# Performance work log

Measured on AMD Instinct MI355X. Metric: run time of the kernel, lower is better.

Reference implementation:

```python
import jax, jax.numpy as jnp
import numpy as np

N = 50000          # nodes
E = 800000         # edges (before self-loops)
NIN = 300          # n_in
H = 4              # heads
C = 64             # nhid (per-head out channels)
G = 256            # number of graphs in batch
NOUT = 768         # nout
NEG_SLOPE_ATT = 0.2   # PyG GATConv leaky-relu slope for attention logits
NEG_SLOPE_ACT = 0.01  # nn.LeakyReLU default


def setup_inputs() -> dict:
    key = jax.random.key(0)
    ks = jax.random.split(key, 9)
    x = jax.random.normal(ks[0], (N, NIN), dtype=jnp.float32)
    edge_index = jax.random.randint(ks[1], (2, E), 0, N, dtype=jnp.int32)
    batch = jnp.sort(jax.random.randint(ks[2], (N,), 0, G, dtype=jnp.int32))
    lin_w = jax.random.normal(ks[3], (NIN, H * C), dtype=jnp.float32) / np.sqrt(NIN)
    att_src = jax.random.normal(ks[4], (H, C), dtype=jnp.float32) / np.sqrt(C)
    att_dst = jax.random.normal(ks[5], (H, C), dtype=jnp.float32) / np.sqrt(C)
    bias = jnp.zeros((H * C,), dtype=jnp.float32)
    fc1_w = jax.random.normal(ks[6], (H * C, NOUT), dtype=jnp.float32) / np.sqrt(H * C)
    fc1_b = jnp.zeros((NOUT,), dtype=jnp.float32)
    return {"x": x, "edge_index": edge_index, "batch": batch, "lin_w": lin_w,
            "att_src": att_src, "att_dst": att_dst, "bias": bias,
            "fc1_w": fc1_w, "fc1_b": fc1_b}


def reference(x, edge_index, batch, lin_w, att_src, att_dst, bias, fc1_w, fc1_b):
    n = x.shape[0]
    h = (x @ lin_w).reshape(n, H, C)                      # [N,H,C]
    # add self-loops (PyG GATConv default)
    loop = jnp.arange(n, dtype=edge_index.dtype)
    src = jnp.concatenate([edge_index[0], loop])          # [E+N]
    dst = jnp.concatenate([edge_index[1], loop])
    # per-edge attention logits
    a_src = jnp.einsum('nhc,hc->nh', h, att_src)          # [N,H]
    a_dst = jnp.einsum('nhc,hc->nh', h, att_dst)
    e = jax.nn.leaky_relu(a_src[src] + a_dst[dst], NEG_SLOPE_ATT)  # [E+N,H]
    # segment softmax grouped by destination node (self-loops -> every segment nonempty)
    emax = jax.ops.segment_max(e, dst, num_segments=n)    # [N,H]
    ee = jnp.exp(e - emax[dst])
    denom = jax.ops.segment_sum(ee, dst, num_segments=n)
    alpha = ee / denom[dst]                               # [E+N,H]
    # weighted message aggregation
    msg = h[src] * alpha[..., None]                       # [E+N,H,C]
    out = jax.ops.segment_sum(msg, dst, num_segments=n).reshape(n, H * C) + bias
    out = jax.nn.leaky_relu(out, NEG_SLOPE_ACT)
    # global mean pool over graphs
    sums = jax.ops.segment_sum(out, batch, num_segments=G)        # [G,H*C]
    cnt = jax.ops.segment_sum(jnp.ones((n, 1), out.dtype), batch, num_segments=G)
    pooled = sums / jnp.maximum(cnt, 1.0)
    return pooled @ fc1_w + fc1_b                         # [G,NOUT]
```

## Files before the change

kernel.cpp:

```cpp
#include <hip/hip_runtime.h>
#include <hip/hip_bf16.h>

using bf16 = __hip_bfloat16;
typedef __attribute__((ext_vector_type(8))) short short8;
typedef __attribute__((ext_vector_type(4))) float f32x4;

constexpr int N   = 50000;
constexpr int E   = 800000;
constexpr int NIN = 300;
constexpr int H   = 4;
constexpr int C   = 64;
constexpr int HC  = H * C;
constexpr int G   = 256;
constexpr int NOUT = 768;
constexpr int NKB = 10;
constexpr int NT  = 782;
constexpr int DCAP = 64;
constexpr int SCB  = (E + 255) / 256;

__device__ __forceinline__ float b2f(bf16 v) { return __bfloat162float(v); }
__device__ __forceinline__ float us2f(unsigned short u) {
    bf16 b; *(unsigned short*)&b = u; return __bfloat162float(b);
}
__device__ __forceinline__ unsigned short f2us(float f) {
    bf16 b = __float2bfloat16(f); return *(unsigned short*)&b;
}
__device__ __forceinline__ float lrelu_att(float v) { return v > 0.f ? v : 0.2f * v; }
__device__ __forceinline__ float lrelu_act(float v) { return v > 0.f ? v : 0.01f * v; }
__device__ __forceinline__ float ldin(const void* p, int isbf, size_t i) {
    return isbf ? b2f(((const bf16*)p)[i]) : ((const float*)p)[i];
}
__device__ __forceinline__ short8 pack8u(ushort4 lo, ushort4 hi) {
    short8 r;
    r[0] = (short)lo.x; r[1] = (short)lo.y; r[2] = (short)lo.z; r[3] = (short)lo.w;
    r[4] = (short)hi.x; r[5] = (short)hi.y; r[6] = (short)hi.z; r[7] = (short)hi.w;
    return r;
}
__device__ __forceinline__ short8 pack8f(float4 lo, float4 hi) {
    short8 r;
    r[0] = (short)f2us(lo.x); r[1] = (short)f2us(lo.y); r[2] = (short)f2us(lo.z); r[3] = (short)f2us(lo.w);
    r[4] = (short)f2us(hi.x); r[5] = (short)f2us(hi.y); r[6] = (short)f2us(hi.z); r[7] = (short)f2us(hi.w);
    return r;
}

__device__ __forceinline__ short8 loadA_bf(const unsigned short* __restrict__ xr, int kb, int q) {
    ushort4 z = make_ushort4(0, 0, 0, 0);
    ushort4 lo = z, hi = z;
    if (kb < 9) {
        lo = *(const ushort4*)(xr + kb * 32);
        hi = *(const ushort4*)(xr + kb * 32 + 4);
    } else if (q == 0) {
        lo = *(const ushort4*)(xr + 288); hi = *(const ushort4*)(xr + 292);
    } else if (q == 1) {
        lo = *(const ushort4*)(xr + 288);
    }
    return pack8u(lo, hi);
}
__device__ __forceinline__ short8 loadA_f32(const float* __restrict__ xf, int kb, int q) {
    float4 zf = make_float4(0.f, 0.f, 0.f, 0.f);
    float4 lo = zf, hi = zf;
    if (kb < 9) {
        lo = *(const float4*)(xf + kb * 32);
        hi = *(const float4*)(xf + kb * 32 + 4);
    } else if (q == 0) {
        lo = *(const float4*)(xf + 288); hi = *(const float4*)(xf + 292);
    } else if (q == 1) {
        lo = *(const float4*)(xf + 288);
    }
    return pack8f(lo, hi);
}

__device__ __forceinline__ int block_detect(const unsigned short* __restrict__ xr) {
    __shared__ int cnt_s;
    if (threadIdx.x == 0) cnt_s = 0;
    __syncthreads();
    unsigned short u = xr[threadIdx.x & 255];
    int ex = (u >> 7) & 0xFF;
    int ok = (ex == 0) || (ex >= 100 && ex <= 140);
    if (threadIdx.x < 256) atomicAdd(&cnt_s, ok);
    __syncthreads();
    return (cnt_s >= 240) ? 1 : 0;
}

__global__ __launch_bounds__(256) void k_pre(const unsigned short* __restrict__ xr,
                                             const void* __restrict__ w,
                                             const int* __restrict__ batch,
                                             int* __restrict__ flag,
                                             unsigned short* __restrict__ bswz,
                                             int* __restrict__ gs,
                                             const int* __restrict__ ei,
                                             int* __restrict__ cnt,
                                             int* __restrict__ csrB) {
    int b = blockIdx.x;
    if (b < 40) {
        int isbf = block_detect(xr);
        if (b == 0 && threadIdx.x == 0) *flag = isbf;
        int fb = b * 4 + (threadIdx.x >> 6);
        if (fb < 160) {
            int kb = fb >> 4, nb = fb & 15;
            int lane = threadIdx.x & 63;
            int q = lane >> 4, cl = lane & 15;
            int n = nb * 16 + cl;
            unsigned short v[8];
#pragma unroll
            for (int j = 0; j < 8; j++) {
                int k = kb * 32 + q * 8 + j;
                float f = (k < NIN) ? ldin(w, isbf, (size_t)k * HC + n) : 0.f;
                v[j] = f2us(f);
            }
            ushort4* dst = (ushort4*)(bswz + ((size_t)fb * 64 + lane) * 8);
            dst[0] = make_ushort4(v[0], v[1], v[2], v[3]);
            dst[1] = make_ushort4(v[4], v[5], v[6], v[7]);
        }
    } else if (b == 40) {
        int g = threadIdx.x;
        int lo = 0, hi = N;
        while (lo < hi) {
            int mid = (lo + hi) >> 1;
            if (batch[mid] < g) lo = mid + 1;
            else hi = mid;
        }
        gs[g] = lo;
        if (g == 0) gs[G] = N;
    } else {
        int e = (b - 41) * 256 + threadIdx.x;
        if (e < E) {
            int s = ei[e], d = ei[E + e];
            int pos = atomicAdd(&cnt[d], 1);
            if (pos < DCAP) csrB[(size_t)d * DCAP + pos] = s;
        }
    }
}

__global__ __launch_bounds__(256, 4) void k_lin4(const void* __restrict__ x,
                                                 const unsigned short* __restrict__ bswz,
                                                 const void* __restrict__ att_s,
                                                 const void* __restrict__ att_d,
                                                 unsigned short* __restrict__ hb,
                                                 float* __restrict__ a_src,
                                                 float* __restrict__ a_dst,
                                                 const int* __restrict__ flag) {
    __shared__ unsigned short bs[40 * 64 * 8];
    int isbf = *flag;
    int t = threadIdx.x;
    int c       = blockIdx.x & 7;
    int j       = blockIdx.x >> 3;
    int quarter = j & 3;
    int bslot   = (j >> 2) * 8 + c;
    for (int i = t; i < 40 * 64; i += 256) {
        int f = i >> 6, lane = i & 63;
        int kb = f >> 2, nbl = f & 3;
        const int4* src = (const int4*)(bswz + ((size_t)(kb * 16 + quarter * 4 + nbl) * 64 + lane) * 8);
        ((int4*)bs)[i] = *src;
    }
    __syncthreads();

    int wave = t >> 6, lane = t & 63;
    int q = lane >> 4, cl = lane & 15;
    int hh = quarter;
    float as_h[4], ad_h[4];
#pragma unroll
    for (int nbl = 0; nbl < 4; nbl++) {
        as_h[nbl] = ldin(att_s, isbf, (quarter * 4 + nbl) * 16 + cl);
        ad_h[nbl] = ldin(att_d, isbf, (quarter * 4 + nbl) * 16 + cl);
    }
    for (int tile = bslot; tile < NT; tile += 256) {
        int m0 = tile * 64 + wave * 16;
        int row = m0 + cl; if (row >= N) row = N - 1;
        f32x4 acc[4];
#pragma unroll
        for (int nbl = 0; nbl < 4; nbl++) acc[nbl] = f32x4{0.f, 0.f, 0.f, 0.f};
        if (isbf) {
            const unsigned short* xr = (const unsigned short*)x + (size_t)row * NIN + q * 8;
            short8 a_cur = loadA_bf(xr, 0, q);
            short8 a_nxt = loadA_bf(xr, 1, q);
#pragma unroll
            for (int kb = 0; kb < NKB; kb++) {
                short8 a_pf = {};
                if (kb + 2 < NKB) a_pf = loadA_bf(xr, kb + 2, q);
                short8 bfr[4];
#pragma unroll
                for (int nbl = 0; nbl < 4; nbl++)
                    bfr[nbl] = *(const short8*)(bs + ((size_t)(kb * 4 + nbl) * 64 + lane) * 8);
#pragma unroll
                for (int nbl = 0; nbl < 4; nbl++)
                    acc[nbl] = __builtin_amdgcn_mfma_f32_16x16x32_bf16(a_cur, bfr[nbl], acc[nbl], 0, 0, 0);
                a_cur = a_nxt; a_nxt = a_pf;
            }
        } else {
            const float* xf = (const float*)x + (size_t)row * NIN + q * 8;
            short8 a_cur = loadA_f32(xf, 0, q);
            short8 a_nxt = loadA_f32(xf, 1, q);
#pragma unroll
            for (int kb = 0; kb < NKB; kb++) {
                short8 a_pf = {};
                if (kb + 2 < NKB) a_pf = loadA_f32(xf, kb + 2, q);
                short8 bfr[4];
#pragma unroll
                for (int nbl = 0; nbl < 4; nbl++)
                    bfr[nbl] = *(const short8*)(bs + ((size_t)(kb * 4 + nbl) * 64 + lane) * 8);
#pragma unroll
                for (int nbl = 0; nbl < 4; nbl++)
                    acc[nbl] = __builtin_amdgcn_mfma_f32_16x16x32_bf16(a_cur, bfr[nbl], acc[nbl], 0, 0, 0);
                a_cur = a_nxt; a_nxt = a_pf;
            }
        }
        float ps[4], pd[4];
#pragma unroll
        for (int r = 0; r < 4; r++) { ps[r] = 0.f; pd[r] = 0.f; }
#pragma unroll
        for (int nbl = 0; nbl < 4; nbl++) {
            int nb = quarter * 4 + nbl;
#pragma unroll
            for (int r = 0; r < 4; r++) {
                float v = acc[nbl][r];
                ps[r] += v * as_h[nbl];
                pd[r] += v * ad_h[nbl];
                int gm = m0 + q * 4 + r;
                if (gm < N) hb[(size_t)gm * HC + nb * 16 + cl] = f2us(v);
            }
        }
#pragma unroll
        for (int r = 0; r < 4; r++) {
            float vs = ps[r], vd = pd[r];
#pragma unroll
            for (int m = 1; m < 16; m <<= 1) {
                vs += __shfl_xor(vs, m, 64);
                vd += __shfl_xor(vd, m, 64);
            }
            int gm = m0 + q * 4 + r;
            if (cl == 0 && gm < N) {
                a_src[gm * 4 + hh] = vs;
                a_dst[gm * 4 + hh] = vd;
            }
        }
    }
}

__global__ __launch_bounds__(256) void k_agg(const unsigned short* __restrict__ hb,
                                             const float* __restrict__ a_src,
                                             const float* __restrict__ a_dst,
                                             const int* __restrict__ cnt,
                                             const int* __restrict__ csrB,
                                             const void* __restrict__ bias,
                                             unsigned short* __restrict__ outn,
                                             const int* __restrict__ flag) {
    int isbf = *flag;
    int wave = threadIdx.x >> 6, lane = threadIdx.x & 63;
    int n = blockIdx.x * 4 + wave;
    if (n >= N) return;
    int head = lane >> 4;
    float adn = a_dst[n * 4 + head];
    float wself = __expf(lrelu_att(a_src[n * 4 + head] + adn));
    ushort4 hv = *(const ushort4*)&hb[(size_t)n * HC + lane * 4];
    float4 acc;
    acc.x = us2f(hv.x) * wself;
    acc.y = us2f(hv.y) * wself;
    acc.z = us2f(hv.z) * wself;
    acc.w = us2f(hv.w) * wself;
    float ssum = wself;
    int dg = cnt[n]; if (dg > DCAP) dg = DCAP;
    const int* lst = csrB + (size_t)n * DCAP;
    int p0 = 0, p1 = dg;
    int p = p0;
    ushort4 ga0, ga1, ga2, ga3;
    float wa0, wa1, wa2, wa3;
    int ib0 = 0, ib1 = 0, ib2 = 0, ib3 = 0;
    if (p + 4 <= p1) {
        int i0 = lst[p], i1 = lst[p + 1], i2 = lst[p + 2], i3 = lst[p + 3];
        ga0 = *(const ushort4*)&hb[(size_t)i0 * HC + lane * 4];
        ga1 = *(const ushort4*)&hb[(size_t)i1 * HC + lane * 4];
        ga2 = *(const ushort4*)&hb[(size_t)i2 * HC + lane * 4];
        ga3 = *(const ushort4*)&hb[(size_t)i3 * HC + lane * 4];
        wa0 = a_src[(size_t)i0 * 4 + head];
        wa1 = a_src[(size_t)i1 * 4 + head];
        wa2 = a_src[(size_t)i2 * 4 + head];
        wa3 = a_src[(size_t)i3 * 4 + head];
    }
    if (p + 8 <= p1) {
        ib0 = lst[p + 4]; ib1 = lst[p + 5]; ib2 = lst[p + 6]; ib3 = lst[p + 7];
    }
    while (p + 8 <= p1) {
        ushort4 gb0 = *(const ushort4*)&hb[(size_t)ib0 * HC + lane * 4];
        ushort4 gb1 = *(const ushort4*)&hb[(size_t)ib1 * HC + lane * 4];
        ushort4 gb2 = *(const ushort4*)&hb[(size_t)ib2 * HC + lane * 4];
        ushort4 gb3 = *(const ushort4*)&hb[(size_t)ib3 * HC + lane * 4];
        float wb0 = a_src[(size_t)ib0 * 4 + head];
        float wb1 = a_src[(size_t)ib1 * 4 + head];
        float wb2 = a_src[(size_t)ib2 * 4 + head];
        float wb3 = a_src[(size_t)ib3 * 4 + head];
        int ic0 = ib0, ic1 = ib1, ic2 = ib2, ic3 = ib3;
        if (p + 12 <= p1) {
            ic0 = lst[p + 8]; ic1 = lst[p + 9]; ic2 = lst[p + 10]; ic3 = lst[p + 11];
        }
        float e0 = __expf(lrelu_att(wa0 + adn));
        float e1 = __expf(lrelu_att(wa1 + adn));
        float e2 = __expf(lrelu_att(wa2 + adn));
        float e3 = __expf(lrelu_att(wa3 + adn));
        acc.x += us2f(ga0.x) * e0 + us2f(ga1.x) * e1 + us2f(ga2.x) * e2 + us2f(ga3.x) * e3;
        acc.y += us2f(ga0.y) * e0 + us2f(ga1.y) * e1 + us2f(ga2.y) * e2 + us2f(ga3.y) * e3;
        acc.z += us2f(ga0.z) * e0 + us2f(ga1.z) * e1 + us2f(ga2.z) * e2 + us2f(ga3.z) * e3;
        acc.w += us2f(ga0.w) * e0 + us2f(ga1.w) * e1 + us2f(ga2.w) * e2 + us2f(ga3.w) * e3;
        ssum += (e0 + e1) + (e2 + e3);
        ga0 = gb0; ga1 = gb1; ga2 = gb2; ga3 = gb3;
        wa0 = wb0; wa1 = wb1; wa2 = wb2; wa3 = wb3;
        ib0 = ic0; ib1 = ic1; ib2 = ic2; ib3 = ic3;
        p += 4;
    }
    if (p + 4 <= p1) {
        float e0 = __expf(lrelu_att(wa0 + adn));
        float e1 = __expf(lrelu_att(wa1 + adn));
        float e2 = __expf(lrelu_att(wa2 + adn));
        float e3 = __expf(lrelu_att(wa3 + adn));
        acc.x += us2f(ga0.x) * e0 + us2f(ga1.x) * e1 + us2f(ga2.x) * e2 + us2f(ga3.x) * e3;
        acc.y += us2f(ga0.y) * e0 + us2f(ga1.y) * e1 + us2f(ga2.y) * e2 + us2f(ga3.y) * e3;
        acc.z += us2f(ga0.z) * e0 + us2f(ga1.z) * e1 + us2f(ga2.z) * e2 + us2f(ga3.z) * e3;
        acc.w += us2f(ga0.w) * e0 + us2f(ga1.w) * e1 + us2f(ga2.w) * e2 + us2f(ga3.w) * e3;
        ssum += (e0 + e1) + (e2 + e3);
        p += 4;
    }
    for (; p < p1; p++) {
        int s = lst[p];
        float wv = __expf(lrelu_att(a_src[(size_t)s * 4 + head] + adn));
        ushort4 hs = *(const ushort4*)&hb[(size_t)s * HC + lane * 4];
        acc.x += us2f(hs.x) * wv;
        acc.y += us2f(hs.y) * wv;
        acc.z += us2f(hs.z) * wv;
        acc.w += us2f(hs.w) * wv;
        ssum += wv;
    }
    float inv = 1.f / ssum;
    ushort4 o;
    o.x = f2us(lrelu_act(acc.x * inv + ldin(bias, isbf, lane * 4 + 0)));
    o.y = f2us(lrelu_act(acc.y * inv + ldin(bias, isbf, lane * 4 + 1)));
    o.z = f2us(lrelu_act(acc.z * inv + ldin(bias, isbf, lane * 4 + 2)));
    o.w = f2us(lrelu_act(acc.w * inv + ldin(bias, isbf, lane * 4 + 3)));
    *(ushort4*)&outn[(size_t)n * HC + lane * 4] = o;
}

__global__ __launch_bounds__(1024) void k_fcp(const unsigned short* __restrict__ outn,
                                              const int* __restrict__ gs,
                                              const void* __restrict__ fw,
                                              const void* __restrict__ fb,
                                              void* __restrict__ out,
                                              const int* __restrict__ flag) {
    __shared__ float pl4[4][HC];
    __shared__ float pl[HC];
    int isbf = *flag;
    int g = blockIdx.x, t = threadIdx.x;
    int qq = t >> 8, ch = t & 255;
    int s = gs[g], e2 = gs[g + 1];
    int len = e2 - s;
    int r0 = s + (len * qq) / 4;
    int r1 = s + (len * (qq + 1)) / 4;
    float a0 = 0.f, a1 = 0.f, a2 = 0.f, a3 = 0.f;
    int r = r0;
    for (; r + 4 <= r1; r += 4) {
        a0 += us2f(outn[(size_t)(r + 0) * HC + ch]);
        a1 += us2f(outn[(size_t)(r + 1) * HC + ch]);
        a2 += us2f(outn[(size_t)(r + 2) * HC + ch]);
        a3 += us2f(outn[(size_t)(r + 3) * HC + ch]);
    }
    for (; r < r1; r++) a0 += us2f(outn[(size_t)r * HC + ch]);
    pl4[qq][ch] = (a0 + a1) + (a2 + a3);
    __syncthreads();
    if (t < HC) {
        float inv = 1.f / (float)(len > 1 ? len : 1);
        pl[t] = (pl4[0][t] + pl4[1][t] + pl4[2][t] + pl4[3][t]) * inv;
    }
    __syncthreads();
    if (t < NOUT) {
        float acc = ldin(fb, isbf, t);
#pragma unroll 8
        for (int k = 0; k < HC; k++) acc += pl[k] * ldin(fw, isbf, (size_t)k * NOUT + t);
        size_t oi = (size_t)g * NOUT + t;
        if (isbf) ((bf16*)out)[oi] = __float2bfloat16(acc);
        else      ((float*)out)[oi] = acc;
    }
}

extern "C" void kernel_launch(void* const* d_in, const int* in_sizes, int n_in,
                              void* d_out, int out_size, void* d_ws, size_t ws_size,
                              hipStream_t stream) {
    const void* x     = d_in[0];
    const int*  ei    = (const int*)d_in[1];
    const int*  batch = (const int*)d_in[2];
    const void* lin_w = d_in[3];
    const void* att_s = d_in[4];
    const void* att_d = d_in[5];
    const void* bias  = d_in[6];
    const void* fc1w  = d_in[7];
    const void* fc1b  = d_in[8];

    char* p = (char*)d_ws;
    unsigned short* hb   = (unsigned short*)p; p += (size_t)N * HC * 2;
    unsigned short* outn = (unsigned short*)p; p += (size_t)N * HC * 2;
    float* a_src  = (float*)p; p += (size_t)N * H * 4;
    float* a_dst  = (float*)p; p += (size_t)N * H * 4;
    int* cnt      = (int*)p;   p += (size_t)N * 4;
    int* csrB     = (int*)p;   p += (size_t)N * DCAP * 4;
    unsigned short* bswz = (unsigned short*)p; p += (size_t)160 * 64 * 8 * 2;
    int* gs       = (int*)p;   p += (size_t)(G + 4) * 4;
    int* flag     = (int*)p;   p += 16;

    hipMemsetAsync(cnt, 0, (size_t)N * 4, stream);
    k_pre<<<41 + SCB, 256, 0, stream>>>((const unsigned short*)x, lin_w, batch,
                                        flag, bswz, gs, ei, cnt, csrB);
    k_lin4<<<1024, 256, 0, stream>>>(x, bswz, att_s, att_d, hb, a_src, a_dst, flag);
    k_agg<<<(N + 3) / 4, 256, 0, stream>>>(hb, a_src, a_dst, cnt, csrB, bias, outn, flag);
    k_fcp<<<G, 1024, 0, stream>>>(outn, gs, fc1w, fc1b, d_out, flag);
}
```

Baseline: 275.6 us.

## Fold preprocessing kernel into linear and pooling kernels to drop a launch

Removes the separate k_pre kernel. Each linear-projection block now builds its swizzled bf16 weight slice in shared memory straight from lin_w, and also runs its own format detection. The edge bucketing (atomic count plus CSR scatter) is appended to the end of the same kernel, with each block taking 782 edges. The graph-boundary binary search moves into the pooling kernel. This saves one kernel launch and the intermediate buffers, in exchange for redundant weight conversion and detection work in every block and a serialized scatter tail after the GEMM.

```diff
diff --git a/kernel.cpp b/kernel.cpp
--- a/kernel.cpp
+++ b/kernel.cpp
@@ -16,7 +16,7 @@
 constexpr int NKB = 10;
 constexpr int NT  = 782;
 constexpr int DCAP = 64;
-constexpr int SCB  = (E + 255) / 256;
+constexpr int EPB  = 782;
 
 __device__ __forceinline__ float b2f(bf16 v) { return __bfloat162float(v); }
 __device__ __forceinline__ float us2f(unsigned short u) {
@@ -82,67 +82,21 @@
     return (cnt_s >= 240) ? 1 : 0;
 }
 
-__global__ __launch_bounds__(256) void k_pre(const unsigned short* __restrict__ xr,
-                                             const void* __restrict__ w,
-                                             const int* __restrict__ batch,
-                                             int* __restrict__ flag,
-                                             unsigned short* __restrict__ bswz,
-                                             int* __restrict__ gs,
-                                             const int* __restrict__ ei,
-                                             int* __restrict__ cnt,
-                                             int* __restrict__ csrB) {
-    int b = blockIdx.x;
-    if (b < 40) {
-        int isbf = block_detect(xr);
-        if (b == 0 && threadIdx.x == 0) *flag = isbf;
-        int fb = b * 4 + (threadIdx.x >> 6);
-        if (fb < 160) {
-            int kb = fb >> 4, nb = fb & 15;
-            int lane = threadIdx.x & 63;
-            int q = lane >> 4, cl = lane & 15;
-            int n = nb * 16 + cl;
-            unsigned short v[8];
-#pragma unroll
-            for (int j = 0; j < 8; j++) {
-                int k = kb * 32 + q * 8 + j;
-                float f = (k < NIN) ? ldin(w, isbf, (size_t)k * HC + n) : 0.f;
-                v[j] = f2us(f);
-            }
-            ushort4* dst = (ushort4*)(bswz + ((size_t)fb * 64 + lane) * 8);
-            dst[0] = make_ushort4(v[0], v[1], v[2], v[3]);
-            dst[1] = make_ushort4(v[4], v[5], v[6], v[7]);
-        }
-    } else if (b == 40) {
-        int g = threadIdx.x;
-        int lo = 0, hi = N;
-        while (lo < hi) {
-            int mid = (lo + hi) >> 1;
-            if (batch[mid] < g) lo = mid + 1;
-            else hi = mid;
-        }
-        gs[g] = lo;
-        if (g == 0) gs[G] = N;
-    } else {
-        int e = (b - 41) * 256 + threadIdx.x;
-        if (e < E) {
-            int s = ei[e], d = ei[E + e];
-            int pos = atomicAdd(&cnt[d], 1);
-            if (pos < DCAP) csrB[(size_t)d * DCAP + pos] = s;
-        }
-    }
-}
-
-__global__ __launch_bounds__(256, 4) void k_lin4(const void* __restrict__ x,
-                                                 const unsigned short* __restrict__ bswz,
+__global__ __launch_bounds__(256, 4) void k_main(const void* __restrict__ x,
+                                                 const void* __restrict__ lin_w,
                                                  const void* __restrict__ att_s,
                                                  const void* __restrict__ att_d,
                                                  unsigned short* __restrict__ hb,
                                                  float* __restrict__ a_src,
                                                  float* __restrict__ a_dst,
-                                                 const int* __restrict__ flag) {
+                                                 int* __restrict__ flag,
+                                                 const int* __restrict__ ei,
+                                                 int* __restrict__ cnt,
+                                                 int* __restrict__ csrB) {
     __shared__ unsigned short bs[40 * 64 * 8];
-    int isbf = *flag;
     int t = threadIdx.x;
+    int isbf = block_detect((const unsigned short*)x);
+    if (blockIdx.x == 0 && t == 0) *flag = isbf;
     int c       = blockIdx.x & 7;
     int j       = blockIdx.x >> 3;
     int quarter = j & 3;
@@ -150,8 +104,19 @@
     for (int i = t; i < 40 * 64; i += 256) {
         int f = i >> 6, lane = i & 63;
         int kb = f >> 2, nbl = f & 3;
-        const int4* src = (const int4*)(bswz + ((size_t)(kb * 16 + quarter * 4 + nbl) * 64 + lane) * 8);
-        ((int4*)bs)[i] = *src;
+        int nb = quarter * 4 + nbl;
+        int q = lane >> 4, cl = lane & 15;
+        int n = nb * 16 + cl;
+        unsigned short v[8];
+#pragma unroll
+        for (int jj = 0; jj < 8; jj++) {
+            int k = kb * 32 + q * 8 + jj;
+            float fv = (k < NIN) ? ldin(lin_w, isbf, (size_t)k * HC + n) : 0.f;
+            v[jj] = f2us(fv);
+        }
+        ushort4* dst = (ushort4*)(bs + (size_t)i * 8);
+        dst[0] = make_ushort4(v[0], v[1], v[2], v[3]);
+        dst[1] = make_ushort4(v[4], v[5], v[6], v[7]);
     }
     __syncthreads();
 
@@ -233,6 +198,15 @@
                 a_src[gm * 4 + hh] = vs;
                 a_dst[gm * 4 + hh] = vd;
             }
+        }
+    }
+
+    for (int i = t; i < EPB; i += 256) {
+        int e = blockIdx.x * EPB + i;
+        if (e < E) {
+            int s = ei[e], d = ei[E + e];
+            int pos = atomicAdd(&cnt[d], 1);
+            if (pos < DCAP) csrB[(size_t)d * DCAP + pos] = s;
         }
     }
 }
@@ -339,17 +313,29 @@
 }
 
 __global__ __launch_bounds__(1024) void k_fcp(const unsigned short* __restrict__ outn,
-                                              const int* __restrict__ gs,
+                                              const int* __restrict__ batch,
                                               const void* __restrict__ fw,
                                               const void* __restrict__ fb,
                                               void* __restrict__ out,
                                               const int* __restrict__ flag) {
     __shared__ float pl4[4][HC];
     __shared__ float pl[HC];
+    __shared__ int sse[2];
     int isbf = *flag;
     int g = blockIdx.x, t = threadIdx.x;
+    if (t < 2) {
+        int tgt = g + t;
+        int lo = 0, hi = N;
+        while (lo < hi) {
+            int mid = (lo + hi) >> 1;
+            if (batch[mid] < tgt) lo = mid + 1;
+            else hi = mid;
+        }
+        sse[t] = lo;
+    }
+    __syncthreads();
+    int s = sse[0], e2 = sse[1];
     int qq = t >> 8, ch = t & 255;
-    int s = gs[g], e2 = gs[g + 1];
     int len = e2 - s;
     int r0 = s + (len * qq) / 4;
     int r1 = s + (len * (qq + 1)) / 4;
@@ -399,14 +385,11 @@
     float* a_dst  = (float*)p; p += (size_t)N * H * 4;
     int* cnt      = (int*)p;   p += (size_t)N * 4;
     int* csrB     = (int*)p;   p += (size_t)N * DCAP * 4;
-    unsigned short* bswz = (unsigned short*)p; p += (size_t)160 * 64 * 8 * 2;
-    int* gs       = (int*)p;   p += (size_t)(G + 4) * 4;
     int* flag     = (int*)p;   p += 16;
 
     hipMemsetAsync(cnt, 0, (size_t)N * 4, stream);
-    k_pre<<<41 + SCB, 256, 0, stream>>>((const unsigned short*)x, lin_w, batch,
-                                        flag, bswz, gs, ei, cnt, csrB);
-    k_lin4<<<1024, 256, 0, stream>>>(x, bswz, att_s, att_d, hb, a_src, a_dst, flag);
+    k_main<<<1024, 256, 0, stream>>>(x, lin_w, att_s, att_d, hb, a_src, a_dst,
+                                     flag, ei, cnt, csrB);
     k_agg<<<(N + 3) / 4, 256, 0, stream>>>(hb, a_src, a_dst, cnt, csrB, bias, outn, flag);
-    k_fcp<<<G, 1024, 0, stream>>>(outn, gs, fc1w, fc1b, d_out, flag);
-}
+    k_fcp<<<G, 1024, 0, stream>>>(outn, batch, fc1w, fc1b, d_out, flag);
+}
```

Result: slower. 313.7 us (+13.8%).
